# Kernel tuning notes

Measured on AMD Instinct MI355X. Metric: run time of the kernel, lower is better.

The kernel has to match this reference:

```python
import jax, jax.numpy as jnp
import numpy as np

N, E, F_IN, H, OUT, G = 40000, 640000, 128, 128, 10, 256


def setup_inputs() -> dict:
    key = jax.random.key(0)
    ks = jax.random.split(key, 8)
    x = jax.random.normal(ks[0], (N, F_IN), dtype=jnp.float32)
    edge_index = jax.random.randint(ks[1], (2, E), 0, N, dtype=jnp.int32)
    batch = jnp.sort(jax.random.randint(ks[2], (N,), 0, G, dtype=jnp.int32))
    W1 = jax.random.normal(ks[3], (F_IN, H), dtype=jnp.float32) / np.sqrt(F_IN)
    b1 = jnp.zeros((H,), dtype=jnp.float32)
    W2 = jax.random.normal(ks[4], (H, H), dtype=jnp.float32) / np.sqrt(H)
    b2 = jnp.zeros((H,), dtype=jnp.float32)
    Wfc = jax.random.normal(ks[5], (H, OUT), dtype=jnp.float32) / np.sqrt(H)
    bfc = jnp.zeros((OUT,), dtype=jnp.float32)
    return {"x": x, "edge_index": edge_index, "batch": batch,
            "W1": W1, "b1": b1, "W2": W2, "b2": b2, "Wfc": Wfc, "bfc": bfc}


def _gcn_conv(x, W, b, row, col, num_nodes):
    # x' = D^{-1/2} (A+I) D^{-1/2} (x W) + b   (self-loops already in row/col)
    xw = x @ W                                            # [N, H]
    ones = jnp.ones(row.shape[0], dtype=x.dtype)
    deg = jax.ops.segment_sum(ones, col, num_segments=num_nodes)
    dinv = jnp.where(deg > 0, jax.lax.rsqrt(jnp.maximum(deg, 1.0)), 0.0)
    norm = dinv[row] * dinv[col]                          # [E+N]
    msg = xw[row] * norm[:, None]                         # gather + scale
    return jax.ops.segment_sum(msg, col, num_segments=num_nodes) + b


def reference(x, edge_index, batch, W1, b1, W2, b2, Wfc, bfc):
    num_nodes = x.shape[0]
    loop = jnp.arange(num_nodes, dtype=edge_index.dtype)
    row = jnp.concatenate([edge_index[0], loop])
    col = jnp.concatenate([edge_index[1], loop])

    h = jax.nn.relu(_gcn_conv(x, W1, b1, row, col, num_nodes))
    h = jax.nn.relu(_gcn_conv(h, W2, b2, row, col, num_nodes))

    # global_mean_pool over graph ids
    sums = jax.ops.segment_sum(h, batch, num_segments=G)  # [G, H]
    cnt = jax.ops.segment_sum(jnp.ones(num_nodes, h.dtype), batch, num_segments=G)
    pooled = sums / jnp.maximum(cnt, 1.0)[:, None]

    logits = pooled @ Wfc + bfc                           # [G, OUT]
    return jax.nn.log_softmax(logits, axis=-1)
```

## Files before the change

### kernel.cpp

```cpp
#include <hip/hip_runtime.h>
#include <math.h>

#define H_DIM 128
#define OUT_DIM 10

typedef __attribute__((ext_vector_type(8))) __bf16 bf16x8;
typedef __attribute__((ext_vector_type(8))) unsigned short ushort8;
typedef __attribute__((ext_vector_type(4))) float f32x4;

__device__ inline unsigned short f2bf_rne(float f) {
    unsigned int u = __float_as_uint(f);
    unsigned int r = u + 0x7FFFu + ((u >> 16) & 1u);
    return (unsigned short)(r >> 16);
}
__device__ inline float bf_lo(unsigned int u) { return __uint_as_float(u << 16); }
__device__ inline float bf_hi(unsigned int u) { return __uint_as_float(u & 0xFFFF0000u); }

__global__ __launch_bounds__(256) void prep_kernel(const float* __restrict__ W1,
                                                   const float* __restrict__ W2,
                                                   unsigned short* __restrict__ Wt1Hi,
                                                   unsigned short* __restrict__ Wt1Lo,
                                                   unsigned short* __restrict__ Wt2Hi,
                                                   unsigned short* __restrict__ Wt2Lo,
                                                   int hb,
                                                   const int* __restrict__ col,
                                                   int* __restrict__ cnt,
                                                   int* __restrict__ rank, int E) {
    if (blockIdx.x < (unsigned)hb) {
        int e = blockIdx.x * 256 + threadIdx.x;
        if (e < E) rank[e] = atomicAdd(&cnt[col[e]], 1);
    } else {
        int i = (blockIdx.x - hb) * 256 + threadIdx.x;
        const float* src   = (i < 16384) ? W1    : W2;
        unsigned short* dh = (i < 16384) ? Wt1Hi : Wt2Hi;
        unsigned short* dl = (i < 16384) ? Wt1Lo : Wt2Lo;
        int idx = i & 16383;
        int k = idx >> 7, n = idx & 127;
        float v = src[idx];
        unsigned short hbv = f2bf_rne(v);
        float hf = __uint_as_float((unsigned int)hbv << 16);
        unsigned short lb = f2bf_rne(v - hf);
        dh[n * H_DIM + k] = hbv;
        dl[n * H_DIM + k] = lb;
    }
}

__global__ __launch_bounds__(256) void scan_phase1(const int* __restrict__ cnt,
                                                   int* __restrict__ blockSums,
                                                   float* __restrict__ dinv, int N) {
    __shared__ int red[256];
    int base = blockIdx.x * 1024;
    int t = threadIdx.x;
    int s = 0;
    for (int i = 0; i < 4; ++i) {
        int idx = base + t * 4 + i;
        if (idx < N) {
            int cv = cnt[idx];
            s += cv;
            dinv[idx] = rsqrtf((float)cv + 1.0f);
        }
    }
    red[t] = s;
    __syncthreads();
    for (int d = 128; d > 0; d >>= 1) {
        if (t < d) red[t] += red[t + d];
        __syncthreads();
    }
    if (t == 0) blockSums[blockIdx.x] = red[0];
}

__global__ __launch_bounds__(256) void scan_phase23(const int* __restrict__ cnt,
                                                    const int* __restrict__ blockSums,
                                                    int* __restrict__ offs, int N, int B) {
    __shared__ int red[256];
    __shared__ int bsum[256];
    int base = blockIdx.x * 1024;
    int t = threadIdx.x;

    bsum[t] = (t < B && t < (int)blockIdx.x) ? blockSums[t] : 0;

    int v[4];
    int s = 0;
    for (int i = 0; i < 4; ++i) {
        int idx = base + t * 4 + i;
        v[i] = (idx < N) ? cnt[idx] : 0;
        s += v[i];
    }
    red[t] = s;
    __syncthreads();
    for (int d = 128; d > 0; d >>= 1) {
        if (t < d) bsum[t] += bsum[t + d];
        __syncthreads();
    }
    for (int d = 1; d < 256; d <<= 1) {
        int x = (t >= d) ? red[t - d] : 0;
        __syncthreads();
        red[t] += x;
        __syncthreads();
    }
    int run = bsum[0] + ((t == 0) ? 0 : red[t - 1]);
    for (int i = 0; i < 4; ++i) {
        int idx = base + t * 4 + i;
        if (idx < N) { offs[idx] = run; run += v[i]; }
    }
    if ((int)blockIdx.x == B - 1 && t == 255) offs[N] = run;
}

__global__ __launch_bounds__(256) void scatter_gemm1(
        const int* __restrict__ row, const int* __restrict__ col,
        const int* __restrict__ rank, const float* __restrict__ dinv,
        const int* __restrict__ offs, int2* __restrict__ csr, int E, int sb,
        const float* __restrict__ Xf,
        const unsigned short* __restrict__ WtHi, const unsigned short* __restrict__ WtLo,
        unsigned short* __restrict__ Yb, int N) {
    if (blockIdx.x < (unsigned)sb) {
        int e = blockIdx.x * 256 + threadIdx.x;
        if (e >= E) return;
        int r = row[e], c = col[e], rk = rank[e];
        int pos = offs[c] + rk;
        int2 p; p.x = r; p.y = __float_as_int(dinv[r] * dinv[c]);
        csr[pos] = p;
        return;
    }
    int blk  = blockIdx.x - sb;
    int lane = threadIdx.x & 63;
    int wv   = threadIdx.x >> 6;
    int m16  = lane & 15;
    int quad = lane >> 4;
    int nodeBase = blk * 32;

    f32x4 acc[2][2] = {};

    #pragma unroll
    for (int kt = 0; kt < 4; ++kt) {
        int k0 = kt * 32 + quad * 8;

        ushort8 aHi[2], aLo[2];
        #pragma unroll
        for (int mi = 0; mi < 2; ++mi) {
            int node = nodeBase + mi * 16 + m16;
            if (node >= N) node = N - 1;
            const float* p = Xf + (size_t)node * H_DIM + k0;
            f32x4 u = *(const f32x4*)p;
            f32x4 w = *(const f32x4*)(p + 4);
            float vv[8] = {u.x, u.y, u.z, u.w, w.x, w.y, w.z, w.w};
            #pragma unroll
            for (int j = 0; j < 8; ++j) {
                unsigned short hbv = f2bf_rne(vv[j]);
                aHi[mi][j] = hbv;
                aLo[mi][j] = f2bf_rne(vv[j] - __uint_as_float((unsigned int)hbv << 16));
            }
        }

        ushort8 bHi[2], bLo[2];
        #pragma unroll
        for (int ni = 0; ni < 2; ++ni) {
            int n = (wv * 2 + ni) * 16 + m16;
            size_t off = (size_t)n * H_DIM + k0;
            bHi[ni] = *(const ushort8*)(WtHi + off);
            bLo[ni] = *(const ushort8*)(WtLo + off);
        }

        #pragma unroll
        for (int mi = 0; mi < 2; ++mi)
            #pragma unroll
            for (int ni = 0; ni < 2; ++ni) {
                acc[mi][ni] = __builtin_amdgcn_mfma_f32_16x16x32_bf16(
                    __builtin_bit_cast(bf16x8, aHi[mi]),
                    __builtin_bit_cast(bf16x8, bHi[ni]), acc[mi][ni], 0, 0, 0);
                acc[mi][ni] = __builtin_amdgcn_mfma_f32_16x16x32_bf16(
                    __builtin_bit_cast(bf16x8, aLo[mi]),
                    __builtin_bit_cast(bf16x8, bHi[ni]), acc[mi][ni], 0, 0, 0);
                acc[mi][ni] = __builtin_amdgcn_mfma_f32_16x16x32_bf16(
                    __builtin_bit_cast(bf16x8, aHi[mi]),
                    __builtin_bit_cast(bf16x8, bLo[ni]), acc[mi][ni], 0, 0, 0);
            }
    }

    #pragma unroll
    for (int mi = 0; mi < 2; ++mi)
        #pragma unroll
        for (int r = 0; r < 4; ++r) {
            int node = nodeBase + mi * 16 + quad * 4 + r;
            if (node < N) {
                #pragma unroll
                for (int ni = 0; ni < 2; ++ni) {
                    int c = (wv * 2 + ni) * 16 + m16;
                    Yb[(size_t)node * H_DIM + c] = f2bf_rne(acc[mi][ni][r]);
                }
            }
        }
}

__global__ __launch_bounds__(256) void gemm_mfma_bf16A(const unsigned short* __restrict__ Xb,
                                                       const unsigned short* __restrict__ WtHi,
                                                       const unsigned short* __restrict__ WtLo,
                                                       unsigned short* __restrict__ Yb, int N) {
    int lane = threadIdx.x & 63;
    int wv   = threadIdx.x >> 6;
    int m16  = lane & 15;
    int quad = lane >> 4;
    int nodeBase = blockIdx.x * 32;

    f32x4 acc[2][2] = {};

    #pragma unroll
    for (int kt = 0; kt < 4; ++kt) {
        int k0 = kt * 32 + quad * 8;

        ushort8 a[2];
        #pragma unroll
        for (int mi = 0; mi < 2; ++mi) {
            int node = nodeBase + mi * 16 + m16;
            if (node >= N) node = N - 1;
            a[mi] = *(const ushort8*)(Xb + (size_t)node * H_DIM + k0);
        }

        ushort8 bHi[2], bLo[2];
        #pragma unroll
        for (int ni = 0; ni < 2; ++ni) {
            int n = (wv * 2 + ni) * 16 + m16;
            size_t off = (size_t)n * H_DIM + k0;
            bHi[ni] = *(const ushort8*)(WtHi + off);
            bLo[ni] = *(const ushort8*)(WtLo + off);
        }

        #pragma unroll
        for (int mi = 0; mi < 2; ++mi)
            #pragma unroll
            for (int ni = 0; ni < 2; ++ni) {
                acc[mi][ni] = __builtin_amdgcn_mfma_f32_16x16x32_bf16(
                    __builtin_bit_cast(bf16x8, a[mi]),
                    __builtin_bit_cast(bf16x8, bHi[ni]), acc[mi][ni], 0, 0, 0);
                acc[mi][ni] = __builtin_amdgcn_mfma_f32_16x16x32_bf16(
                    __builtin_bit_cast(bf16x8, a[mi]),
                    __builtin_bit_cast(bf16x8, bLo[ni]), acc[mi][ni], 0, 0, 0);
            }
    }

    #pragma unroll
    for (int mi = 0; mi < 2; ++mi)
        #pragma unroll
        for (int r = 0; r < 4; ++r) {
            int node = nodeBase + mi * 16 + quad * 4 + r;
            if (node < N) {
                #pragma unroll
                for (int ni = 0; ni < 2; ++ni) {
                    int c = (wv * 2 + ni) * 16 + m16;
                    Yb[(size_t)node * H_DIM + c] = f2bf_rne(acc[mi][ni][r]);
                }
            }
        }
}

template <int POOL>
__global__ __launch_bounds__(256) void agg_fused_t(const unsigned short* __restrict__ XWb,
                                                   const float* __restrict__ dinv,
                                                   const int2* __restrict__ csr,
                                                   const int* __restrict__ offs,
                                                   const float* __restrict__ bias,
                                                   unsigned short* __restrict__ OUTb,
                                                   const int* __restrict__ batch,
                                                   float* __restrict__ pooledSum, int N) {
    int wave = (blockIdx.x * 256 + threadIdx.x) >> 6;
    int lane = threadIdx.x & 63;
    int wv   = threadIdx.x >> 6;
    bool active = wave < N;
    if (!POOL && !active) return;

    float ax = 0.f, ay = 0.f;
    int c = wave;
    if (active) {
        int start = offs[c], end = offs[c + 1];
        float dc = dinv[c];
        const unsigned int* XW32 = (const unsigned int*)XWb;

        float ax0, ay0;
        {
            unsigned int u = XW32[(size_t)c * 64 + lane];
            float s = dc * dc;
            ax0 = bf_lo(u) * s; ay0 = bf_hi(u) * s;
        }
        float ax1 = 0.f, ay1 = 0.f, ax2 = 0.f, ay2 = 0.f, ax3 = 0.f, ay3 = 0.f;

        for (int base = start; base < end; base += 64) {
            int m = end - base; if (m > 64) m = 64;
            int2 ce; ce.x = 0; ce.y = 0;
            if (lane < m) ce = csr[base + lane];

            int j = 0;
            for (; j + 3 < m; j += 4) {
                int r0 = __shfl(ce.x, j);     int b0 = __shfl(ce.y, j);
                int r1 = __shfl(ce.x, j + 1); int b1 = __shfl(ce.y, j + 1);
                int r2 = __shfl(ce.x, j + 2); int b2 = __shfl(ce.y, j + 2);
                int r3 = __shfl(ce.x, j + 3); int b3 = __shfl(ce.y, j + 3);
                unsigned int g0 = XW32[(size_t)r0 * 64 + lane];
                unsigned int g1 = XW32[(size_t)r1 * 64 + lane];
                unsigned int g2 = XW32[(size_t)r2 * 64 + lane];
                unsigned int g3 = XW32[(size_t)r3 * 64 + lane];
                float n0 = __int_as_float(b0);
                float n1 = __int_as_float(b1);
                float n2 = __int_as_float(b2);
                float n3 = __int_as_float(b3);
                ax0 += bf_lo(g0) * n0; ay0 += bf_hi(g0) * n0;
                ax1 += bf_lo(g1) * n1; ay1 += bf_hi(g1) * n1;
                ax2 += bf_lo(g2) * n2; ay2 += bf_hi(g2) * n2;
                ax3 += bf_lo(g3) * n3; ay3 += bf_hi(g3) * n3;
            }
            for (; j < m; ++j) {
                int r = __shfl(ce.x, j); int b = __shfl(ce.y, j);
                unsigned int g = XW32[(size_t)r * 64 + lane];
                float nrm = __int_as_float(b);
                ax1 += bf_lo(g) * nrm; ay1 += bf_hi(g) * nrm;
            }
        }
        ax = (ax0 + ax1) + (ax2 + ax3);
        ay = (ay0 + ay1) + (ay2 + ay3);
        float2 b = ((const float2*)bias)[lane];
        ax = fmaxf(ax + b.x, 0.f);
        ay = fmaxf(ay + b.y, 0.f);
    }

    if constexpr (!POOL) {
        unsigned int o = (unsigned int)f2bf_rne(ax) | ((unsigned int)f2bf_rne(ay) << 16);
        ((unsigned int*)(OUTb + (size_t)c * H_DIM))[lane] = o;
        return;
    } else {
        __shared__ float lacc[4][H_DIM];
        __shared__ int lg[4];
        if (lane == 0) lg[wv] = active ? batch[c] : -1;
        float2 t2; t2.x = ax; t2.y = ay;
        ((float2*)(&lacc[wv][0]))[lane] = t2;
        __syncthreads();
        int t = threadIdx.x;
        if (t < H_DIM) {
            float s = 0.f; int cur = -1;
            #pragma unroll
            for (int w = 0; w < 4; ++w) {
                int g = lg[w];
                if (g < 0) continue;
                if (g != cur) {
                    if (cur >= 0) atomicAdd(&pooledSum[cur * H_DIM + t], s);
                    s = 0.f; cur = g;
                }
                s += lacc[w][t];
            }
            if (cur >= 0) atomicAdd(&pooledSum[cur * H_DIM + t], s);
        }
    }
}

__global__ __launch_bounds__(64) void head_kernel(const float* __restrict__ pooledSum,
                                                  const int* __restrict__ batch,
                                                  const float* __restrict__ Wfc,
                                                  const float* __restrict__ bfc,
                                                  float* __restrict__ out, int N) {
    __shared__ float sl[OUT_DIM + 2];
    __shared__ int bounds[2];
    int g = blockIdx.x;
    int j = threadIdx.x;
    if (j < 2) {
        int v = g + j;
        int lo = 0, hi = N;
        while (lo < hi) {
            int mid = (lo + hi) >> 1;
            if (batch[mid] < v) lo = mid + 1; else hi = mid;
        }
        bounds[j] = lo;
    }
    __syncthreads();
    int cnt = bounds[1] - bounds[0];
    float inv = 1.0f / (float)(cnt > 0 ? cnt : 1);
    if (j < OUT_DIM) {
        float acc = 0.f;
        const float* p = pooledSum + g * H_DIM;
        for (int k = 0; k < H_DIM; ++k) acc += p[k] * Wfc[k * OUT_DIM + j];
        sl[j] = acc * inv + bfc[j];
    }
    __syncthreads();
    if (j == 0) {
        float m = sl[0];
        for (int i = 1; i < OUT_DIM; ++i) m = fmaxf(m, sl[i]);
        float s = 0.f;
        for (int i = 0; i < OUT_DIM; ++i) s += expf(sl[i] - m);
        sl[OUT_DIM] = m + logf(s);
    }
    __syncthreads();
    if (j < OUT_DIM) out[g * OUT_DIM + j] = sl[j] - sl[OUT_DIM];
}

extern "C" void kernel_launch(void* const* d_in, const int* in_sizes, int n_in,
                              void* d_out, int out_size, void* d_ws, size_t ws_size,
                              hipStream_t stream) {
    const float* x     = (const float*)d_in[0];
    const int*   ei    = (const int*)  d_in[1];
    const int*   batch = (const int*)  d_in[2];
    const float* W1    = (const float*)d_in[3];
    const float* b1    = (const float*)d_in[4];
    const float* W2    = (const float*)d_in[5];
    const float* b2    = (const float*)d_in[6];
    const float* Wfc   = (const float*)d_in[7];
    const float* bfc   = (const float*)d_in[8];
    float* out = (float*)d_out;

    int N = in_sizes[2];
    int E = in_sizes[1] / 2;
    int G = out_size / OUT_DIM;
    const int* row = ei;
    const int* col = ei + E;

    char* wsb = (char*)d_ws;
    size_t nAlign = (size_t)((N + 256) / 256) * 256;
    size_t eAlign = (size_t)((E + 255) / 256) * 256;
    int*   cnt       = (int*)wsb;
    float* pooledSum = (float*)(cnt + nAlign);
    int*   offs      = (int*)(pooledSum + (size_t)G * H_DIM);
    int*   rank      = offs + nAlign;
    float* dinv      = (float*)(rank + eAlign);
    int2*  csr       = (int2*)(dinv + nAlign);
    unsigned short* Xb = (unsigned short*)(csr + E);
    unsigned short* Hb = Xb + (size_t)N * H_DIM;
    int* blockSums = (int*)(Hb + (size_t)N * H_DIM);
    unsigned short* Wt1Hi = (unsigned short*)(blockSums + 256);
    unsigned short* Wt1Lo = Wt1Hi + H_DIM * H_DIM;
    unsigned short* Wt2Hi = Wt1Lo + H_DIM * H_DIM;
    unsigned short* Wt2Lo = Wt2Hi + H_DIM * H_DIM;

    int scanBlocks = (N + 1023) / 1024;
    int histBlocks = (E + 255) / 256;
    int gemmBlocks = (N + 31) / 32;

    hipMemsetAsync(cnt, 0, (nAlign + (size_t)G * H_DIM) * sizeof(int), stream);

    prep_kernel<<<histBlocks + 128, 256, 0, stream>>>(
        W1, W2, Wt1Hi, Wt1Lo, Wt2Hi, Wt2Lo, histBlocks, col, cnt, rank, E);

    scan_phase1<<<scanBlocks, 256, 0, stream>>>(cnt, blockSums, dinv, N);
    scan_phase23<<<scanBlocks, 256, 0, stream>>>(cnt, blockSums, offs, N, scanBlocks);

    scatter_gemm1<<<histBlocks + gemmBlocks, 256, 0, stream>>>(
        row, col, rank, dinv, offs, csr, E, histBlocks,
        x, Wt1Hi, Wt1Lo, Xb, N);

    int aggBlocks = (N + 3) / 4;

    agg_fused_t<0><<<aggBlocks, 256, 0, stream>>>(Xb, dinv, csr, offs, b1, Hb,
                                                  nullptr, nullptr, N);

    gemm_mfma_bf16A<<<gemmBlocks, 256, 0, stream>>>(Hb, Wt2Hi, Wt2Lo, Xb, N);

    agg_fused_t<1><<<aggBlocks, 256, 0, stream>>>(Xb, dinv, csr, offs, b2, nullptr,
                                                  batch, pooledSum, N);

    head_kernel<<<G, 64, 0, stream>>>(pooledSum, batch, Wfc, bfc, out, N);
}
```

Before: 230.3 us.

## Fuse layer-1 aggregation with layer-2 GEMM via shared-memory tile, unroll gathers by 8

Layer-1 neighbour aggregation and the layer-2 MFMA GEMM now run in one kernel. Each block aggregates 16 nodes into a shared-memory bf16 tile and immediately multiplies it by W2, which removes a full N×128 intermediate write and read plus one launch. The edge-gather loops in both aggregation kernels are unrolled to 8 to keep more loads in flight. The cost is less parallelism: each wave now walks 4 nodes serially, and the weight loads are amortised over 16 rows instead of 32.

```diff
diff --git a/kernel.cpp b/kernel.cpp
--- a/kernel.cpp
+++ b/kernel.cpp
@@ -192,81 +192,145 @@
         }
 }
 
-__global__ __launch_bounds__(256) void gemm_mfma_bf16A(const unsigned short* __restrict__ Xb,
-                                                       const unsigned short* __restrict__ WtHi,
-                                                       const unsigned short* __restrict__ WtLo,
-                                                       unsigned short* __restrict__ Yb, int N) {
+__global__ __launch_bounds__(256) void agg1_gemm2(
+        const unsigned short* __restrict__ XWb,
+        const float* __restrict__ dinv,
+        const int2* __restrict__ csr,
+        const int* __restrict__ offs,
+        const float* __restrict__ bias,
+        const unsigned short* __restrict__ WtHi,
+        const unsigned short* __restrict__ WtLo,
+        unsigned short* __restrict__ Yb,
+        int N) {
+    __shared__ unsigned short hrow[16][136];
     int lane = threadIdx.x & 63;
     int wv   = threadIdx.x >> 6;
+    int nodeBase = blockIdx.x * 16;
+    const unsigned int* XW32 = (const unsigned int*)XWb;
+    float2 bv = ((const float2*)bias)[lane];
+
+    for (int i = 0; i < 4; ++i) {
+        int c = nodeBase + wv * 4 + i;
+        float ax = 0.f, ay = 0.f;
+        if (c < N) {
+            int start = offs[c], end = offs[c + 1];
+            float dc = dinv[c];
+            float ax0, ay0;
+            {
+                unsigned int u = XW32[(size_t)c * 64 + lane];
+                float s = dc * dc;
+                ax0 = bf_lo(u) * s; ay0 = bf_hi(u) * s;
+            }
+            float ax1 = 0.f, ay1 = 0.f, ax2 = 0.f, ay2 = 0.f, ax3 = 0.f, ay3 = 0.f;
+
+            for (int base = start; base < end; base += 64) {
+                int m = end - base; if (m > 64) m = 64;
+                int2 ce; ce.x = 0; ce.y = 0;
+                if (lane < m) ce = csr[base + lane];
+
+                int j = 0;
+                for (; j + 7 < m; j += 8) {
+                    int r0 = __shfl(ce.x, j);     int b0 = __shfl(ce.y, j);
+                    int r1 = __shfl(ce.x, j + 1); int b1 = __shfl(ce.y, j + 1);
+                    int r2 = __shfl(ce.x, j + 2); int b2 = __shfl(ce.y, j + 2);
+                    int r3 = __shfl(ce.x, j + 3); int b3 = __shfl(ce.y, j + 3);
+                    int r4 = __shfl(ce.x, j + 4); int b4 = __shfl(ce.y, j + 4);
+                    int r5 = __shfl(ce.x, j + 5); int b5 = __shfl(ce.y, j + 5);
+                    int r6 = __shfl(ce.x, j + 6); int b6 = __shfl(ce.y, j + 6);
+                    int r7 = __shfl(ce.x, j + 7); int b7 = __shfl(ce.y, j + 7);
+                    unsigned int g0 = XW32[(size_t)r0 * 64 + lane];
+                    unsigned int g1 = XW32[(size_t)r1 * 64 + lane];
+                    unsigned int g2 = XW32[(size_t)r2 * 64 + lane];
+                    unsigned int g3 = XW32[(size_t)r3 * 64 + lane];
+                    unsigned int g4 = XW32[(size_t)r4 * 64 + lane];
+                    unsigned int g5 = XW32[(size_t)r5 * 64 + lane];
+                    unsigned int g6 = XW32[(size_t)r6 * 64 + lane];
+                    unsigned int g7 = XW32[(size_t)r7 * 64 + lane];
+                    ax0 += bf_lo(g0) * __int_as_float(b0); ay0 += bf_hi(g0) * __int_as_float(b0);
+                    ax1 += bf_lo(g1) * __int_as_float(b1); ay1 += bf_hi(g1) * __int_as_float(b1);
+                    ax2 += bf_lo(g2) * __int_as_float(b2); ay2 += bf_hi(g2) * __int_as_float(b2);
+                    ax3 += bf_lo(g3) * __int_as_float(b3); ay3 += bf_hi(g3) * __int_as_float(b3);
+                    ax0 += bf_lo(g4) * __int_as_float(b4); ay0 += bf_hi(g4) * __int_as_float(b4);
+                    ax1 += bf_lo(g5) * __int_as_float(b5); ay1 += bf_hi(g5) * __int_as_float(b5);
+                    ax2 += bf_lo(g6) * __int_as_float(b6); ay2 += bf_hi(g6) * __int_as_float(b6);
+                    ax3 += bf_lo(g7) * __int_as_float(b7); ay3 += bf_hi(g7) * __int_as_float(b7);
+                }
+                for (; j + 3 < m; j += 4) {
+                    int r0 = __shfl(ce.x, j);     int b0 = __shfl(ce.y, j);
+                    int r1 = __shfl(ce.x, j + 1); int b1 = __shfl(ce.y, j + 1);
+                    int r2 = __shfl(ce.x, j + 2); int b2 = __shfl(ce.y, j + 2);
+                    int r3 = __shfl(ce.x, j + 3); int b3 = __shfl(ce.y, j + 3);
+                    unsigned int g0 = XW32[(size_t)r0 * 64 + lane];
+                    unsigned int g1 = XW32[(size_t)r1 * 64 + lane];
+                    unsigned int g2 = XW32[(size_t)r2 * 64 + lane];
+                    unsigned int g3 = XW32[(size_t)r3 * 64 + lane];
+                    ax0 += bf_lo(g0) * __int_as_float(b0); ay0 += bf_hi(g0) * __int_as_float(b0);
+                    ax1 += bf_lo(g1) * __int_as_float(b1); ay1 += bf_hi(g1) * __int_as_float(b1);
+                    ax2 += bf_lo(g2) * __int_as_float(b2); ay2 += bf_hi(g2) * __int_as_float(b2);
+                    ax3 += bf_lo(g3) * __int_as_float(b3); ay3 += bf_hi(g3) * __int_as_float(b3);
+                }
+                for (; j < m; ++j) {
+                    int r = __shfl(ce.x, j); int b = __shfl(ce.y, j);
+                    unsigned int g = XW32[(size_t)r * 64 + lane];
+                    float nrm = __int_as_float(b);
+                    ax1 += bf_lo(g) * nrm; ay1 += bf_hi(g) * nrm;
+                }
+            }
+            ax = (ax0 + ax1) + (ax2 + ax3);
+            ay = (ay0 + ay1) + (ay2 + ay3);
+            ax = fmaxf(ax + bv.x, 0.f);
+            ay = fmaxf(ay + bv.y, 0.f);
+        }
+        unsigned int o = (unsigned int)f2bf_rne(ax) | ((unsigned int)f2bf_rne(ay) << 16);
+        *(unsigned int*)&hrow[wv * 4 + i][lane * 2] = o;
+    }
+    __syncthreads();
+
     int m16  = lane & 15;
     int quad = lane >> 4;
-    int nodeBase = blockIdx.x * 32;
-
-    f32x4 acc[2][2] = {};
-
+    f32x4 acc[2] = {};
     #pragma unroll
     for (int kt = 0; kt < 4; ++kt) {
         int k0 = kt * 32 + quad * 8;
-
-        ushort8 a[2];
-        #pragma unroll
-        for (int mi = 0; mi < 2; ++mi) {
-            int node = nodeBase + mi * 16 + m16;
-            if (node >= N) node = N - 1;
-            a[mi] = *(const ushort8*)(Xb + (size_t)node * H_DIM + k0);
-        }
-
-        ushort8 bHi[2], bLo[2];
+        ushort8 a = *(const ushort8*)&hrow[m16][k0];
         #pragma unroll
         for (int ni = 0; ni < 2; ++ni) {
             int n = (wv * 2 + ni) * 16 + m16;
             size_t off = (size_t)n * H_DIM + k0;
-            bHi[ni] = *(const ushort8*)(WtHi + off);
-            bLo[ni] = *(const ushort8*)(WtLo + off);
-        }
-
-        #pragma unroll
-        for (int mi = 0; mi < 2; ++mi)
+            ushort8 bHi = *(const ushort8*)(WtHi + off);
+            ushort8 bLo = *(const ushort8*)(WtLo + off);
+            acc[ni] = __builtin_amdgcn_mfma_f32_16x16x32_bf16(
+                __builtin_bit_cast(bf16x8, a),
+                __builtin_bit_cast(bf16x8, bHi), acc[ni], 0, 0, 0);
+            acc[ni] = __builtin_amdgcn_mfma_f32_16x16x32_bf16(
+                __builtin_bit_cast(bf16x8, a),
+                __builtin_bit_cast(bf16x8, bLo), acc[ni], 0, 0, 0);
+        }
+    }
+    #pragma unroll
+    for (int r = 0; r < 4; ++r) {
+        int node = nodeBase + quad * 4 + r;
+        if (node < N) {
             #pragma unroll
             for (int ni = 0; ni < 2; ++ni) {
-                acc[mi][ni] = __builtin_amdgcn_mfma_f32_16x16x32_bf16(
-                    __builtin_bit_cast(bf16x8, a[mi]),
-                    __builtin_bit_cast(bf16x8, bHi[ni]), acc[mi][ni], 0, 0, 0);
-                acc[mi][ni] = __builtin_amdgcn_mfma_f32_16x16x32_bf16(
-                    __builtin_bit_cast(bf16x8, a[mi]),
-                    __builtin_bit_cast(bf16x8, bLo[ni]), acc[mi][ni], 0, 0, 0);
-            }
-    }
-
-    #pragma unroll
-    for (int mi = 0; mi < 2; ++mi)
-        #pragma unroll
-        for (int r = 0; r < 4; ++r) {
-            int node = nodeBase + mi * 16 + quad * 4 + r;
-            if (node < N) {
-                #pragma unroll
-                for (int ni = 0; ni < 2; ++ni) {
-                    int c = (wv * 2 + ni) * 16 + m16;
-                    Yb[(size_t)node * H_DIM + c] = f2bf_rne(acc[mi][ni][r]);
-                }
-            }
-        }
-}
-
-template <int POOL>
-__global__ __launch_bounds__(256) void agg_fused_t(const unsigned short* __restrict__ XWb,
-                                                   const float* __restrict__ dinv,
-                                                   const int2* __restrict__ csr,
-                                                   const int* __restrict__ offs,
-                                                   const float* __restrict__ bias,
-                                                   unsigned short* __restrict__ OUTb,
-                                                   const int* __restrict__ batch,
-                                                   float* __restrict__ pooledSum, int N) {
+                int cc = (wv * 2 + ni) * 16 + m16;
+                Yb[(size_t)node * H_DIM + cc] = f2bf_rne(acc[ni][r]);
+            }
+        }
+    }
+}
+
+__global__ __launch_bounds__(256) void agg_pool(const unsigned short* __restrict__ XWb,
+                                                const float* __restrict__ dinv,
+                                                const int2* __restrict__ csr,
+                                                const int* __restrict__ offs,
+                                                const float* __restrict__ bias,
+                                                const int* __restrict__ batch,
+                                                float* __restrict__ pooledSum, int N) {
     int wave = (blockIdx.x * 256 + threadIdx.x) >> 6;
     int lane = threadIdx.x & 63;
     int wv   = threadIdx.x >> 6;
     bool active = wave < N;
-    if (!POOL && !active) return;
 
     float ax = 0.f, ay = 0.f;
     int c = wave;
@@ -289,6 +353,32 @@
             if (lane < m) ce = csr[base + lane];
 
             int j = 0;
+            for (; j + 7 < m; j += 8) {
+                int r0 = __shfl(ce.x, j);     int b0 = __shfl(ce.y, j);
+                int r1 = __shfl(ce.x, j + 1); int b1 = __shfl(ce.y, j + 1);
+                int r2 = __shfl(ce.x, j + 2); int b2 = __shfl(ce.y, j + 2);
+                int r3 = __shfl(ce.x, j + 3); int b3 = __shfl(ce.y, j + 3);
+                int r4 = __shfl(ce.x, j + 4); int b4 = __shfl(ce.y, j + 4);
+                int r5 = __shfl(ce.x, j + 5); int b5 = __shfl(ce.y, j + 5);
+                int r6 = __shfl(ce.x, j + 6); int b6 = __shfl(ce.y, j + 6);
+                int r7 = __shfl(ce.x, j + 7); int b7 = __shfl(ce.y, j + 7);
+                unsigned int g0 = XW32[(size_t)r0 * 64 + lane];
+                unsigned int g1 = XW32[(size_t)r1 * 64 + lane];
+                unsigned int g2 = XW32[(size_t)r2 * 64 + lane];
+                unsigned int g3 = XW32[(size_t)r3 * 64 + lane];
+                unsigned int g4 = XW32[(size_t)r4 * 64 + lane];
+                unsigned int g5 = XW32[(size_t)r5 * 64 + lane];
+                unsigned int g6 = XW32[(size_t)r6 * 64 + lane];
+                unsigned int g7 = XW32[(size_t)r7 * 64 + lane];
+                ax0 += bf_lo(g0) * __int_as_float(b0); ay0 += bf_hi(g0) * __int_as_float(b0);
+                ax1 += bf_lo(g1) * __int_as_float(b1); ay1 += bf_hi(g1) * __int_as_float(b1);
+                ax2 += bf_lo(g2) * __int_as_float(b2); ay2 += bf_hi(g2) * __int_as_float(b2);
+                ax3 += bf_lo(g3) * __int_as_float(b3); ay3 += bf_hi(g3) * __int_as_float(b3);
+                ax0 += bf_lo(g4) * __int_as_float(b4); ay0 += bf_hi(g4) * __int_as_float(b4);
+                ax1 += bf_lo(g5) * __int_as_float(b5); ay1 += bf_hi(g5) * __int_as_float(b5);
+                ax2 += bf_lo(g6) * __int_as_float(b6); ay2 += bf_hi(g6) * __int_as_float(b6);
+                ax3 += bf_lo(g7) * __int_as_float(b7); ay3 += bf_hi(g7) * __int_as_float(b7);
+            }
             for (; j + 3 < m; j += 4) {
                 int r0 = __shfl(ce.x, j);     int b0 = __shfl(ce.y, j);
                 int r1 = __shfl(ce.x, j + 1); int b1 = __shfl(ce.y, j + 1);
@@ -298,14 +388,10 @@
                 unsigned int g1 = XW32[(size_t)r1 * 64 + lane];
                 unsigned int g2 = XW32[(size_t)r2 * 64 + lane];
                 unsigned int g3 = XW32[(size_t)r3 * 64 + lane];
-                float n0 = __int_as_float(b0);
-                float n1 = __int_as_float(b1);
-                float n2 = __int_as_float(b2);
-                float n3 = __int_as_float(b3);
-                ax0 += bf_lo(g0) * n0; ay0 += bf_hi(g0) * n0;
-                ax1 += bf_lo(g1) * n1; ay1 += bf_hi(g1) * n1;
-                ax2 += bf_lo(g2) * n2; ay2 += bf_hi(g2) * n2;
-                ax3 += bf_lo(g3) * n3; ay3 += bf_hi(g3) * n3;
+                ax0 += bf_lo(g0) * __int_as_float(b0); ay0 += bf_hi(g0) * __int_as_float(b0);
+                ax1 += bf_lo(g1) * __int_as_float(b1); ay1 += bf_hi(g1) * __int_as_float(b1);
+                ax2 += bf_lo(g2) * __int_as_float(b2); ay2 += bf_hi(g2) * __int_as_float(b2);
+                ax3 += bf_lo(g3) * __int_as_float(b3); ay3 += bf_hi(g3) * __int_as_float(b3);
             }
             for (; j < m; ++j) {
                 int r = __shfl(ce.x, j); int b = __shfl(ce.y, j);
@@ -321,32 +407,26 @@
         ay = fmaxf(ay + b.y, 0.f);
     }
 
-    if constexpr (!POOL) {
-        unsigned int o = (unsigned int)f2bf_rne(ax) | ((unsigned int)f2bf_rne(ay) << 16);
-        ((unsigned int*)(OUTb + (size_t)c * H_DIM))[lane] = o;
-        return;
-    } else {
-        __shared__ float lacc[4][H_DIM];
-        __shared__ int lg[4];
-        if (lane == 0) lg[wv] = active ? batch[c] : -1;
-        float2 t2; t2.x = ax; t2.y = ay;
-        ((float2*)(&lacc[wv][0]))[lane] = t2;
-        __syncthreads();
-        int t = threadIdx.x;
-        if (t < H_DIM) {
-            float s = 0.f; int cur = -1;
-            #pragma unroll
-            for (int w = 0; w < 4; ++w) {
-                int g = lg[w];
-                if (g < 0) continue;
-                if (g != cur) {
-                    if (cur >= 0) atomicAdd(&pooledSum[cur * H_DIM + t], s);
-                    s = 0.f; cur = g;
-                }
-                s += lacc[w][t];
-            }
-            if (cur >= 0) atomicAdd(&pooledSum[cur * H_DIM + t], s);
-        }
+    __shared__ float lacc[4][H_DIM];
+    __shared__ int lg[4];
+    if (lane == 0) lg[wv] = active ? batch[c] : -1;
+    float2 t2; t2.x = ax; t2.y = ay;
+    ((float2*)(&lacc[wv][0]))[lane] = t2;
+    __syncthreads();
+    int t = threadIdx.x;
+    if (t < H_DIM) {
+        float s = 0.f; int cur = -1;
+        #pragma unroll
+        for (int w = 0; w < 4; ++w) {
+            int g = lg[w];
+            if (g < 0) continue;
+            if (g != cur) {
+                if (cur >= 0) atomicAdd(&pooledSum[cur * H_DIM + t], s);
+                s = 0.f; cur = g;
+            }
+            s += lacc[w][t];
+        }
+        if (cur >= 0) atomicAdd(&pooledSum[cur * H_DIM + t], s);
     }
 }
 
@@ -442,15 +522,13 @@
         row, col, rank, dinv, offs, csr, E, histBlocks,
         x, Wt1Hi, Wt1Lo, Xb, N);
 
+    int ag1Blocks = (N + 15) / 16;
+    agg1_gemm2<<<ag1Blocks, 256, 0, stream>>>(Xb, dinv, csr, offs, b1,
+                                              Wt2Hi, Wt2Lo, Hb, N);
+
     int aggBlocks = (N + 3) / 4;
-
-    agg_fused_t<0><<<aggBlocks, 256, 0, stream>>>(Xb, dinv, csr, offs, b1, Hb,
-                                                  nullptr, nullptr, N);
-
-    gemm_mfma_bf16A<<<gemmBlocks, 256, 0, stream>>>(Hb, Wt2Hi, Wt2Lo, Xb, N);
-
-    agg_fused_t<1><<<aggBlocks, 256, 0, stream>>>(Xb, dinv, csr, offs, b2, nullptr,
-                                                  batch, pooledSum, N);
+    agg_pool<<<aggBlocks, 256, 0, stream>>>(Hb, dinv, csr, offs, b2,
+                                            batch, pooledSum, N);
 
     head_kernel<<<G, 64, 0, stream>>>(pooledSum, batch, Wfc, bfc, out, N);
 }
```

Result: no change. 227.4 us (-1.2%).

## Fuse layer-1 aggregation with layer-2 GEMM and split gathers across sub-waves

Applied to the files above, without the earlier changes.

Layer-1 aggregation now writes its 16 node rows into shared memory, and the layer-2 MFMA GEMM runs in the same kernel. This removes one launch and the global round trip of the intermediate hidden matrix. The gather is also changed so each wave splits into four 16-lane groups that each load 16-byte chunks of a different neighbor row, then combine results with xor shuffles. This gives fewer, wider loads per edge, at the cost of extra reduction shuffles and per-block node loops that may limit parallelism.

```diff
diff --git a/kernel.cpp b/kernel.cpp
--- a/kernel.cpp
+++ b/kernel.cpp
@@ -15,6 +15,60 @@
 }
 __device__ inline float bf_lo(unsigned int u) { return __uint_as_float(u << 16); }
 __device__ inline float bf_hi(unsigned int u) { return __uint_as_float(u & 0xFFFF0000u); }
+
+#define ACC4(gv, nv) do { \
+    const unsigned int* _u = (const unsigned int*)&(gv); \
+    ax[0] += bf_lo(_u[0]) * (nv); ay[0] += bf_hi(_u[0]) * (nv); \
+    ax[1] += bf_lo(_u[1]) * (nv); ay[1] += bf_hi(_u[1]) * (nv); \
+    ax[2] += bf_lo(_u[2]) * (nv); ay[2] += bf_hi(_u[2]) * (nv); \
+    ax[3] += bf_lo(_u[3]) * (nv); ay[3] += bf_hi(_u[3]) * (nv); \
+} while (0)
+
+__device__ inline void gather_node(const int4* __restrict__ XW16,
+                                   const int2* __restrict__ csr,
+                                   int start, int end, int c, float dc2,
+                                   int sub, int fl, int lane,
+                                   float ax[4], float ay[4]) {
+    {
+        float s = (sub == 0) ? dc2 : 0.0f;
+        int4 gs = XW16[(size_t)c * 16 + fl];
+        const unsigned int* u = (const unsigned int*)&gs;
+        ax[0] = bf_lo(u[0]) * s; ay[0] = bf_hi(u[0]) * s;
+        ax[1] = bf_lo(u[1]) * s; ay[1] = bf_hi(u[1]) * s;
+        ax[2] = bf_lo(u[2]) * s; ay[2] = bf_hi(u[2]) * s;
+        ax[3] = bf_lo(u[3]) * s; ay[3] = bf_hi(u[3]) * s;
+    }
+    for (int base = start; base < end; base += 64) {
+        int m = end - base; if (m > 64) m = 64;
+        int2 ce; ce.x = c; ce.y = 0;
+        if (lane < m) ce = csr[base + lane];
+        int groups = (m + 3) >> 2;
+        int g = 0;
+        for (; g + 3 < groups; g += 4) {
+            int j = g * 4 + sub;
+            int r0 = __shfl(ce.x, j);      float n0 = __int_as_float(__shfl(ce.y, j));
+            int r1 = __shfl(ce.x, j + 4);  float n1 = __int_as_float(__shfl(ce.y, j + 4));
+            int r2 = __shfl(ce.x, j + 8);  float n2 = __int_as_float(__shfl(ce.y, j + 8));
+            int r3 = __shfl(ce.x, j + 12); float n3 = __int_as_float(__shfl(ce.y, j + 12));
+            int4 g0 = XW16[(size_t)r0 * 16 + fl];
+            int4 g1 = XW16[(size_t)r1 * 16 + fl];
+            int4 g2 = XW16[(size_t)r2 * 16 + fl];
+            int4 g3 = XW16[(size_t)r3 * 16 + fl];
+            ACC4(g0, n0); ACC4(g1, n1); ACC4(g2, n2); ACC4(g3, n3);
+        }
+        for (; g < groups; ++g) {
+            int j = g * 4 + sub;
+            int r = __shfl(ce.x, j); float n = __int_as_float(__shfl(ce.y, j));
+            int4 gg = XW16[(size_t)r * 16 + fl];
+            ACC4(gg, n);
+        }
+    }
+    #pragma unroll
+    for (int q = 0; q < 4; ++q) {
+        ax[q] += __shfl_xor(ax[q], 16); ax[q] += __shfl_xor(ax[q], 32);
+        ay[q] += __shfl_xor(ay[q], 16); ay[q] += __shfl_xor(ay[q], 32);
+    }
+}
 
 __global__ __launch_bounds__(256) void prep_kernel(const float* __restrict__ W1,
                                                    const float* __restrict__ W2,
@@ -192,161 +246,134 @@
         }
 }
 
-__global__ __launch_bounds__(256) void gemm_mfma_bf16A(const unsigned short* __restrict__ Xb,
-                                                       const unsigned short* __restrict__ WtHi,
-                                                       const unsigned short* __restrict__ WtLo,
-                                                       unsigned short* __restrict__ Yb, int N) {
+__global__ __launch_bounds__(256) void agg1_gemm2(
+        const unsigned short* __restrict__ XWb,
+        const float* __restrict__ dinv,
+        const int2* __restrict__ csr,
+        const int* __restrict__ offs,
+        const float* __restrict__ bias,
+        const unsigned short* __restrict__ WtHi,
+        const unsigned short* __restrict__ WtLo,
+        unsigned short* __restrict__ Yb,
+        int N) {
+    __shared__ __align__(16) unsigned short hrow[16][136];
     int lane = threadIdx.x & 63;
     int wv   = threadIdx.x >> 6;
+    int sub  = lane >> 4;
+    int fl   = lane & 15;
+    int nodeBase = blockIdx.x * 16;
+    const int4* XW16 = (const int4*)XWb;
+    float4 b0 = ((const float4*)bias)[fl * 2];
+    float4 b1 = ((const float4*)bias)[fl * 2 + 1];
+
+    for (int i = 0; i < 4; ++i) {
+        int c = nodeBase + wv * 4 + i;
+        float ax[4] = {}, ay[4] = {};
+        if (c < N) {
+            int start = offs[c], end = offs[c + 1];
+            float dc = dinv[c];
+            gather_node(XW16, csr, start, end, c, dc * dc, sub, fl, lane, ax, ay);
+            ax[0] = fmaxf(ax[0] + b0.x, 0.f); ay[0] = fmaxf(ay[0] + b0.y, 0.f);
+            ax[1] = fmaxf(ax[1] + b0.z, 0.f); ay[1] = fmaxf(ay[1] + b0.w, 0.f);
+            ax[2] = fmaxf(ax[2] + b1.x, 0.f); ay[2] = fmaxf(ay[2] + b1.y, 0.f);
+            ax[3] = fmaxf(ax[3] + b1.z, 0.f); ay[3] = fmaxf(ay[3] + b1.w, 0.f);
+        }
+        if (sub == 0) {
+            unsigned int o[4];
+            #pragma unroll
+            for (int q = 0; q < 4; ++q)
+                o[q] = (unsigned int)f2bf_rne(ax[q]) | ((unsigned int)f2bf_rne(ay[q]) << 16);
+            *(int4*)&hrow[wv * 4 + i][fl * 8] = *(const int4*)o;
+        }
+    }
+    __syncthreads();
+
     int m16  = lane & 15;
     int quad = lane >> 4;
-    int nodeBase = blockIdx.x * 32;
-
-    f32x4 acc[2][2] = {};
-
+    f32x4 acc[2] = {};
     #pragma unroll
     for (int kt = 0; kt < 4; ++kt) {
         int k0 = kt * 32 + quad * 8;
-
-        ushort8 a[2];
-        #pragma unroll
-        for (int mi = 0; mi < 2; ++mi) {
-            int node = nodeBase + mi * 16 + m16;
-            if (node >= N) node = N - 1;
-            a[mi] = *(const ushort8*)(Xb + (size_t)node * H_DIM + k0);
-        }
-
-        ushort8 bHi[2], bLo[2];
+        ushort8 a = *(const ushort8*)&hrow[m16][k0];
         #pragma unroll
         for (int ni = 0; ni < 2; ++ni) {
             int n = (wv * 2 + ni) * 16 + m16;
             size_t off = (size_t)n * H_DIM + k0;
-            bHi[ni] = *(const ushort8*)(WtHi + off);
-            bLo[ni] = *(const ushort8*)(WtLo + off);
-        }
-
-        #pragma unroll
-        for (int mi = 0; mi < 2; ++mi)
+            ushort8 bHi = *(const ushort8*)(WtHi + off);
+            ushort8 bLo = *(const ushort8*)(WtLo + off);
+            acc[ni] = __builtin_amdgcn_mfma_f32_16x16x32_bf16(
+                __builtin_bit_cast(bf16x8, a),
+                __builtin_bit_cast(bf16x8, bHi), acc[ni], 0, 0, 0);
+            acc[ni] = __builtin_amdgcn_mfma_f32_16x16x32_bf16(
+                __builtin_bit_cast(bf16x8, a),
+                __builtin_bit_cast(bf16x8, bLo), acc[ni], 0, 0, 0);
+        }
+    }
+    #pragma unroll
+    for (int r = 0; r < 4; ++r) {
+        int node = nodeBase + quad * 4 + r;
+        if (node < N) {
             #pragma unroll
             for (int ni = 0; ni < 2; ++ni) {
-                acc[mi][ni] = __builtin_amdgcn_mfma_f32_16x16x32_bf16(
-                    __builtin_bit_cast(bf16x8, a[mi]),
-                    __builtin_bit_cast(bf16x8, bHi[ni]), acc[mi][ni], 0, 0, 0);
-                acc[mi][ni] = __builtin_amdgcn_mfma_f32_16x16x32_bf16(
-                    __builtin_bit_cast(bf16x8, a[mi]),
-                    __builtin_bit_cast(bf16x8, bLo[ni]), acc[mi][ni], 0, 0, 0);
+                int cc = (wv * 2 + ni) * 16 + m16;
+                Yb[(size_t)node * H_DIM + cc] = f2bf_rne(acc[ni][r]);
             }
-    }
-
-    #pragma unroll
-    for (int mi = 0; mi < 2; ++mi)
-        #pragma unroll
-        for (int r = 0; r < 4; ++r) {
-            int node = nodeBase + mi * 16 + quad * 4 + r;
-            if (node < N) {
-                #pragma unroll
-                for (int ni = 0; ni < 2; ++ni) {
-                    int c = (wv * 2 + ni) * 16 + m16;
-                    Yb[(size_t)node * H_DIM + c] = f2bf_rne(acc[mi][ni][r]);
-                }
-            }
-        }
-}
-
-template <int POOL>
-__global__ __launch_bounds__(256) void agg_fused_t(const unsigned short* __restrict__ XWb,
-                                                   const float* __restrict__ dinv,
-                                                   const int2* __restrict__ csr,
-                                                   const int* __restrict__ offs,
-                                                   const float* __restrict__ bias,
-                                                   unsigned short* __restrict__ OUTb,
-                                                   const int* __restrict__ batch,
-                                                   float* __restrict__ pooledSum, int N) {
+        }
+    }
+}
+
+__global__ __launch_bounds__(256) void agg_pool(const unsigned short* __restrict__ XWb,
+                                                const float* __restrict__ dinv,
+                                                const int2* __restrict__ csr,
+                                                const int* __restrict__ offs,
+                                                const float* __restrict__ bias,
+                                                const int* __restrict__ batch,
+                                                float* __restrict__ pooledSum, int N) {
     int wave = (blockIdx.x * 256 + threadIdx.x) >> 6;
     int lane = threadIdx.x & 63;
     int wv   = threadIdx.x >> 6;
+    int sub  = lane >> 4;
+    int fl   = lane & 15;
     bool active = wave < N;
-    if (!POOL && !active) return;
-
-    float ax = 0.f, ay = 0.f;
+
+    float ax[4] = {}, ay[4] = {};
     int c = wave;
     if (active) {
         int start = offs[c], end = offs[c + 1];
         float dc = dinv[c];
-        const unsigned int* XW32 = (const unsigned int*)XWb;
-
-        float ax0, ay0;
-        {
-            unsigned int u = XW32[(size_t)c * 64 + lane];
-            float s = dc * dc;
-            ax0 = bf_lo(u) * s; ay0 = bf_hi(u) * s;
-        }
-        float ax1 = 0.f, ay1 = 0.f, ax2 = 0.f, ay2 = 0.f, ax3 = 0.f, ay3 = 0.f;
-
-        for (int base = start; base < end; base += 64) {
-            int m = end - base; if (m > 64) m = 64;
-            int2 ce; ce.x = 0; ce.y = 0;
-            if (lane < m) ce = csr[base + lane];
-
-            int j = 0;
-            for (; j + 3 < m; j += 4) {
-                int r0 = __shfl(ce.x, j);     int b0 = __shfl(ce.y, j);
-                int r1 = __shfl(ce.x, j + 1); int b1 = __shfl(ce.y, j + 1);
-                int r2 = __shfl(ce.x, j + 2); int b2 = __shfl(ce.y, j + 2);
-                int r3 = __shfl(ce.x, j + 3); int b3 = __shfl(ce.y, j + 3);
-                unsigned int g0 = XW32[(size_t)r0 * 64 + lane];
-                unsigned int g1 = XW32[(size_t)r1 * 64 + lane];
-                unsigned int g2 = XW32[(size_t)r2 * 64 + lane];
-                unsigned int g3 = XW32[(size_t)r3 * 64 + lane];
-                float n0 = __int_as_float(b0);
-                float n1 = __int_as_float(b1);
-                float n2 = __int_as_float(b2);
-                float n3 = __int_as_float(b3);
-                ax0 += bf_lo(g0) * n0; ay0 += bf_hi(g0) * n0;
-                ax1 += bf_lo(g1) * n1; ay1 += bf_hi(g1) * n1;
-                ax2 += bf_lo(g2) * n2; ay2 += bf_hi(g2) * n2;
-                ax3 += bf_lo(g3) * n3; ay3 += bf_hi(g3) * n3;
+        gather_node((const int4*)XWb, csr, start, end, c, dc * dc, sub, fl, lane, ax, ay);
+        float4 b0 = ((const float4*)bias)[fl * 2];
+        float4 b1 = ((const float4*)bias)[fl * 2 + 1];
+        ax[0] = fmaxf(ax[0] + b0.x, 0.f); ay[0] = fmaxf(ay[0] + b0.y, 0.f);
+        ax[1] = fmaxf(ax[1] + b0.z, 0.f); ay[1] = fmaxf(ay[1] + b0.w, 0.f);
+        ax[2] = fmaxf(ax[2] + b1.x, 0.f); ay[2] = fmaxf(ay[2] + b1.y, 0.f);
+        ax[3] = fmaxf(ax[3] + b1.z, 0.f); ay[3] = fmaxf(ay[3] + b1.w, 0.f);
+    }
+
+    __shared__ float lacc[4][H_DIM];
+    __shared__ int lg[4];
+    if (lane == 0) lg[wv] = active ? batch[c] : -1;
+    if (sub == 0) {
+        float4 f0; f0.x = ax[0]; f0.y = ay[0]; f0.z = ax[1]; f0.w = ay[1];
+        float4 f1; f1.x = ax[2]; f1.y = ay[2]; f1.z = ax[3]; f1.w = ay[3];
+        ((float4*)&lacc[wv][fl * 8])[0] = f0;
+        ((float4*)&lacc[wv][fl * 8])[1] = f1;
+    }
+    __syncthreads();
+    int t = threadIdx.x;
+    if (t < H_DIM) {
+        float s = 0.f; int cur = -1;
+        #pragma unroll
+        for (int w = 0; w < 4; ++w) {
+            int g = lg[w];
+            if (g < 0) continue;
+            if (g != cur) {
+                if (cur >= 0) atomicAdd(&pooledSum[cur * H_DIM + t], s);
+                s = 0.f; cur = g;
             }
-            for (; j < m; ++j) {
-                int r = __shfl(ce.x, j); int b = __shfl(ce.y, j);
-                unsigned int g = XW32[(size_t)r * 64 + lane];
-                float nrm = __int_as_float(b);
-                ax1 += bf_lo(g) * nrm; ay1 += bf_hi(g) * nrm;
-            }
-        }
-        ax = (ax0 + ax1) + (ax2 + ax3);
-        ay = (ay0 + ay1) + (ay2 + ay3);
-        float2 b = ((const float2*)bias)[lane];
-        ax = fmaxf(ax + b.x, 0.f);
-        ay = fmaxf(ay + b.y, 0.f);
-    }
-
-    if constexpr (!POOL) {
-        unsigned int o = (unsigned int)f2bf_rne(ax) | ((unsigned int)f2bf_rne(ay) << 16);
-        ((unsigned int*)(OUTb + (size_t)c * H_DIM))[lane] = o;
-        return;
-    } else {
-        __shared__ float lacc[4][H_DIM];
-        __shared__ int lg[4];
-        if (lane == 0) lg[wv] = active ? batch[c] : -1;
-        float2 t2; t2.x = ax; t2.y = ay;
-        ((float2*)(&lacc[wv][0]))[lane] = t2;
-        __syncthreads();
-        int t = threadIdx.x;
-        if (t < H_DIM) {
-            float s = 0.f; int cur = -1;
-            #pragma unroll
-            for (int w = 0; w < 4; ++w) {
-                int g = lg[w];
-                if (g < 0) continue;
-                if (g != cur) {
-                    if (cur >= 0) atomicAdd(&pooledSum[cur * H_DIM + t], s);
-                    s = 0.f; cur = g;
-                }
-                s += lacc[w][t];
-            }
-            if (cur >= 0) atomicAdd(&pooledSum[cur * H_DIM + t], s);
-        }
+            s += lacc[w][t];
+        }
+        if (cur >= 0) atomicAdd(&pooledSum[cur * H_DIM + t], s);
     }
 }
 
@@ -442,15 +469,13 @@
         row, col, rank, dinv, offs, csr, E, histBlocks,
         x, Wt1Hi, Wt1Lo, Xb, N);
 
+    int ag1Blocks = (N + 15) / 16;
+    agg1_gemm2<<<ag1Blocks, 256, 0, stream>>>(Xb, dinv, csr, offs, b1,
+                                              Wt2Hi, Wt2Lo, Hb, N);
+
     int aggBlocks = (N + 3) / 4;
-
-    agg_fused_t<0><<<aggBlocks, 256, 0, stream>>>(Xb, dinv, csr, offs, b1, Hb,
-                                                  nullptr, nullptr, N);
-
-    gemm_mfma_bf16A<<<gemmBlocks, 256, 0, stream>>>(Hb, Wt2Hi, Wt2Lo, Xb, N);
-
-    agg_fused_t<1><<<aggBlocks, 256, 0, stream>>>(Xb, dinv, csr, offs, b2, nullptr,
-                                                  batch, pooledSum, N);
+    agg_pool<<<aggBlocks, 256, 0, stream>>>(Hb, dinv, csr, offs, b2,
+                                            batch, pooledSum, N);
 
     head_kernel<<<G, 64, 0, stream>>>(pooledSum, batch, Wfc, bfc, out, N);
 }
```

Result: faster. 222.3 us (-3.5%).
